# Kernel optimization log

Measured on AMD Instinct MI355X. Metric: run time of the kernel, lower is better.

## Reference

```python
import jax, jax.numpy as jnp
import numpy as np

N = 1_000_000
C = 128
B = 16  # number of instances (batch segments)
EPS = 1e-5


def setup_inputs() -> dict:
    key = jax.random.key(0)
    k1, k2 = jax.random.split(key)
    x = jax.random.normal(k1, (N, C), dtype=jnp.float32)
    batch_idx = jnp.sort(jax.random.randint(k2, (N,), 0, B, dtype=jnp.int32))
    weight = jnp.ones((1, C), dtype=jnp.float32)
    bias = jnp.zeros((1, C), dtype=jnp.float32)
    return {"x": x, "batch_idx": batch_idx, "weight": weight, "bias": bias}


def reference(x, batch_idx, weight, bias):
    # per-instance counts [B, 1]
    cnt = jax.ops.segment_sum(jnp.ones((x.shape[0], 1), x.dtype), batch_idx,
                              num_segments=B)
    cnt = jnp.maximum(cnt, 1.0)
    # segment mean [B, C]
    mean = jax.ops.segment_sum(x, batch_idx, num_segments=B) / cnt
    centered = x - mean[batch_idx]               # broadcast-add of -mean
    # segment mean of squared centered features -> per-instance variance [B, C]
    var = jax.ops.segment_sum(centered * centered, batch_idx, num_segments=B) / cnt
    instd = 1.0 / jnp.sqrt(var + EPS)            # [B, C]
    # broadcast-multiply, then affine
    return centered * instd[batch_idx] * weight + bias
```

## Files before the change

### kernel.cpp

```cpp
#include <hip/hip_runtime.h>

#define CC 128
#define BSEG 16
#define EPSV 1e-5f
#define ROWS_PER_BLOCK 512

__global__ __launch_bounds__(256) void ms_stats(const float* __restrict__ x,
                                                const int* __restrict__ bidx,
                                                int n,
                                                float* __restrict__ sum,
                                                float* __restrict__ sumsq,
                                                float* __restrict__ cnt)
{
    const int r0 = blockIdx.x * ROWS_PER_BLOCK;
    if (r0 >= n) return;
    const int rend = min(r0 + ROWS_PER_BLOCK, n);
    const int tq = threadIdx.x & 31;
    const int tr = threadIdx.x >> 5;

    const int seg_first = bidx[r0];
    const int seg_last  = bidx[rend - 1];

    float s0 = 0.f, s1 = 0.f, s2 = 0.f, s3 = 0.f;
    float q0 = 0.f, q1 = 0.f, q2 = 0.f, q3 = 0.f;

    if (seg_first == seg_last) {
        for (int r = r0 + tr; r < rend; r += 8) {
            const float4 v = *reinterpret_cast<const float4*>(x + (size_t)r * CC + tq * 4);
            s0 += v.x; s1 += v.y; s2 += v.z; s3 += v.w;
            q0 += v.x * v.x; q1 += v.y * v.y; q2 += v.z * v.z; q3 += v.w * v.w;
        }
        __shared__ float red[8][8][32];
        red[tr][0][tq] = s0; red[tr][1][tq] = s1; red[tr][2][tq] = s2; red[tr][3][tq] = s3;
        red[tr][4][tq] = q0; red[tr][5][tq] = q1; red[tr][6][tq] = q2; red[tr][7][tq] = q3;
        __syncthreads();
        const int j = threadIdx.x >> 5;
        float acc = 0.f;
        #pragma unroll
        for (int k = 0; k < 8; ++k) acc += red[k][j][tq];
        const int ch = tq * 4 + (j & 3);
        atomicAdd(((j < 4) ? sum : sumsq) + seg_first * CC + ch, acc);
        if (threadIdx.x == 0)
            atomicAdd(cnt + seg_first, (float)(rend - r0));
    } else {
        int cur = -1;
        float rows = 0.f;
        for (int r = r0 + tr; r < rend; r += 8) {
            const int seg = bidx[r];
            if (seg != cur) {
                if (cur >= 0) {
                    float* sd = sum   + cur * CC + tq * 4;
                    float* qd = sumsq + cur * CC + tq * 4;
                    atomicAdd(sd + 0, s0); atomicAdd(sd + 1, s1);
                    atomicAdd(sd + 2, s2); atomicAdd(sd + 3, s3);
                    atomicAdd(qd + 0, q0); atomicAdd(qd + 1, q1);
                    atomicAdd(qd + 2, q2); atomicAdd(qd + 3, q3);
                    if (tq == 0) atomicAdd(cnt + cur, rows);
                    s0 = s1 = s2 = s3 = q0 = q1 = q2 = q3 = 0.f;
                    rows = 0.f;
                }
                cur = seg;
            }
            const float4 v = *reinterpret_cast<const float4*>(x + (size_t)r * CC + tq * 4);
            s0 += v.x; s1 += v.y; s2 += v.z; s3 += v.w;
            q0 += v.x * v.x; q1 += v.y * v.y; q2 += v.z * v.z; q3 += v.w * v.w;
            rows += 1.f;
        }
        if (cur >= 0) {
            float* sd = sum   + cur * CC + tq * 4;
            float* qd = sumsq + cur * CC + tq * 4;
            atomicAdd(sd + 0, s0); atomicAdd(sd + 1, s1);
            atomicAdd(sd + 2, s2); atomicAdd(sd + 3, s3);
            atomicAdd(qd + 0, q0); atomicAdd(qd + 1, q1);
            atomicAdd(qd + 2, q2); atomicAdd(qd + 3, q3);
            if (tq == 0) atomicAdd(cnt + cur, rows);
        }
    }
}

__global__ __launch_bounds__(256) void ms_finalize(const float* __restrict__ sum,
                                                   const float* __restrict__ sumsq,
                                                   const float* __restrict__ cnt,
                                                   const float* __restrict__ w,
                                                   const float* __restrict__ bias,
                                                   float* __restrict__ scale,
                                                   float* __restrict__ shift)
{
    const int i = blockIdx.x * blockDim.x + threadIdx.x;
    if (i >= BSEG * CC) return;
    const int b = i / CC;
    const int c = i % CC;
    const float nn = fmaxf(cnt[b], 1.0f);
    const float mean = sum[i] / nn;
    const float var = fmaxf(sumsq[i] / nn - mean * mean, 0.0f);
    const float instd = rsqrtf(var + EPSV);
    const float sc = instd * w[c];
    scale[i] = sc;
    shift[i] = bias[c] - mean * sc;
}

__global__ __launch_bounds__(256) void ms_norm(const float* __restrict__ x,
                                               const int* __restrict__ bidx,
                                               const float* __restrict__ scale,
                                               const float* __restrict__ shift,
                                               float* __restrict__ out,
                                               int n)
{
    __shared__ float4 s_scale[BSEG * 32];
    __shared__ float4 s_shift[BSEG * 32];
    for (int i = threadIdx.x; i < BSEG * 32; i += blockDim.x) {
        s_scale[i] = reinterpret_cast<const float4*>(scale)[i];
        s_shift[i] = reinterpret_cast<const float4*>(shift)[i];
    }
    __syncthreads();

    const unsigned total = (unsigned)n * 32u;
    const unsigned stride = gridDim.x * blockDim.x;
    for (unsigned idx = blockIdx.x * blockDim.x + threadIdx.x; idx < total; idx += stride) {
        const int r = (int)(idx >> 5);
        const int q = (int)(idx & 31);
        const int seg = bidx[r];
        const float4 v  = reinterpret_cast<const float4*>(x)[idx];
        const float4 sc = s_scale[seg * 32 + q];
        const float4 sh = s_shift[seg * 32 + q];
        float4 o;
        o.x = fmaf(v.x, sc.x, sh.x);
        o.y = fmaf(v.y, sc.y, sh.y);
        o.z = fmaf(v.z, sc.z, sh.z);
        o.w = fmaf(v.w, sc.w, sh.w);
        reinterpret_cast<float4*>(out)[idx] = o;
    }
}

extern "C" void kernel_launch(void* const* d_in, const int* in_sizes, int n_in,
                              void* d_out, int out_size, void* d_ws, size_t ws_size,
                              hipStream_t stream)
{
    const float* x    = (const float*)d_in[0];
    const int*   bidx = (const int*)d_in[1];
    const float* w    = (const float*)d_in[2];
    const float* bias = (const float*)d_in[3];
    float* out = (float*)d_out;
    const int n = in_sizes[1];

    float* ws    = (float*)d_ws;
    float* sum   = ws;
    float* sumsq = ws + BSEG * CC;
    float* cnt   = ws + 2 * BSEG * CC;
    float* scale = ws + 2 * BSEG * CC + BSEG;
    float* shift = scale + BSEG * CC;

    hipMemsetAsync(d_ws, 0, (size_t)(2 * BSEG * CC + BSEG) * sizeof(float), stream);

    const int g1 = (n + ROWS_PER_BLOCK - 1) / ROWS_PER_BLOCK;
    ms_stats<<<g1, 256, 0, stream>>>(x, bidx, n, sum, sumsq, cnt);
    ms_finalize<<<(BSEG * CC + 255) / 256, 256, 0, stream>>>(sum, sumsq, cnt, w, bias, scale, shift);
    ms_norm<<<2048, 256, 0, stream>>>(x, bidx, scale, shift, out, n);
}
```

Before: 352.6 us.

## Fuse finalize into norm kernel, reverse traversal, use nontemporal stores

Drops the separate finalize kernel. Each norm block now recomputes the per-segment scale and shift into shared memory from the raw sums, which removes one launch and a global round trip. The norm loop walks rows in reverse so that the most recently read tail of x, likely still in cache after the stats pass, is consumed first. Output is written with nontemporal stores to avoid polluting the cache. The cost is that all 2048 blocks redo the 2048-element finalize, and shared-memory reads become scalar with possible bank conflicts.

```diff
diff --git a/kernel.cpp b/kernel.cpp
--- a/kernel.cpp
+++ b/kernel.cpp
@@ -4,6 +4,8 @@
 #define BSEG 16
 #define EPSV 1e-5f
 #define ROWS_PER_BLOCK 512
+
+typedef float v4f __attribute__((ext_vector_type(4)));
 
 __global__ __launch_bounds__(256) void ms_stats(const float* __restrict__ x,
                                                 const int* __restrict__ bidx,
@@ -26,7 +28,7 @@
 
     if (seg_first == seg_last) {
         for (int r = r0 + tr; r < rend; r += 8) {
-            const float4 v = *reinterpret_cast<const float4*>(x + (size_t)r * CC + tq * 4);
+            const v4f v = *reinterpret_cast<const v4f*>(x + (size_t)r * CC + tq * 4);
             s0 += v.x; s1 += v.y; s2 += v.z; s3 += v.w;
             q0 += v.x * v.x; q1 += v.y * v.y; q2 += v.z * v.z; q3 += v.w * v.w;
         }
@@ -61,7 +63,7 @@
                 }
                 cur = seg;
             }
-            const float4 v = *reinterpret_cast<const float4*>(x + (size_t)r * CC + tq * 4);
+            const v4f v = *reinterpret_cast<const v4f*>(x + (size_t)r * CC + tq * 4);
             s0 += v.x; s1 += v.y; s2 += v.z; s3 += v.w;
             q0 += v.x * v.x; q1 += v.y * v.y; q2 += v.z * v.z; q3 += v.w * v.w;
             rows += 1.f;
@@ -78,57 +80,45 @@
     }
 }
 
-__global__ __launch_bounds__(256) void ms_finalize(const float* __restrict__ sum,
-                                                   const float* __restrict__ sumsq,
-                                                   const float* __restrict__ cnt,
-                                                   const float* __restrict__ w,
-                                                   const float* __restrict__ bias,
-                                                   float* __restrict__ scale,
-                                                   float* __restrict__ shift)
-{
-    const int i = blockIdx.x * blockDim.x + threadIdx.x;
-    if (i >= BSEG * CC) return;
-    const int b = i / CC;
-    const int c = i % CC;
-    const float nn = fmaxf(cnt[b], 1.0f);
-    const float mean = sum[i] / nn;
-    const float var = fmaxf(sumsq[i] / nn - mean * mean, 0.0f);
-    const float instd = rsqrtf(var + EPSV);
-    const float sc = instd * w[c];
-    scale[i] = sc;
-    shift[i] = bias[c] - mean * sc;
-}
-
 __global__ __launch_bounds__(256) void ms_norm(const float* __restrict__ x,
                                                const int* __restrict__ bidx,
-                                               const float* __restrict__ scale,
-                                               const float* __restrict__ shift,
+                                               const float* __restrict__ sum,
+                                               const float* __restrict__ sumsq,
+                                               const float* __restrict__ cnt,
+                                               const float* __restrict__ w,
+                                               const float* __restrict__ bias,
                                                float* __restrict__ out,
                                                int n)
 {
-    __shared__ float4 s_scale[BSEG * 32];
-    __shared__ float4 s_shift[BSEG * 32];
-    for (int i = threadIdx.x; i < BSEG * 32; i += blockDim.x) {
-        s_scale[i] = reinterpret_cast<const float4*>(scale)[i];
-        s_shift[i] = reinterpret_cast<const float4*>(shift)[i];
+    __shared__ float s_scale[BSEG * CC];
+    __shared__ float s_shift[BSEG * CC];
+    for (int i = threadIdx.x; i < BSEG * CC; i += 256) {
+        const int b = i >> 7;
+        const int c = i & (CC - 1);
+        const float nn   = fmaxf(cnt[b], 1.0f);
+        const float mean = sum[i] / nn;
+        const float var  = fmaxf(sumsq[i] / nn - mean * mean, 0.0f);
+        const float sc   = rsqrtf(var + EPSV) * w[c];
+        s_scale[i] = sc;
+        s_shift[i] = fmaf(-mean, sc, bias[c]);
     }
     __syncthreads();
 
-    const unsigned total = (unsigned)n * 32u;
+    const unsigned total  = (unsigned)n * 32u;
     const unsigned stride = gridDim.x * blockDim.x;
-    for (unsigned idx = blockIdx.x * blockDim.x + threadIdx.x; idx < total; idx += stride) {
+    for (unsigned i = blockIdx.x * blockDim.x + threadIdx.x; i < total; i += stride) {
+        const unsigned idx = total - 1u - i;
         const int r = (int)(idx >> 5);
         const int q = (int)(idx & 31);
-        const int seg = bidx[r];
-        const float4 v  = reinterpret_cast<const float4*>(x)[idx];
-        const float4 sc = s_scale[seg * 32 + q];
-        const float4 sh = s_shift[seg * 32 + q];
-        float4 o;
-        o.x = fmaf(v.x, sc.x, sh.x);
-        o.y = fmaf(v.y, sc.y, sh.y);
-        o.z = fmaf(v.z, sc.z, sh.z);
-        o.w = fmaf(v.w, sc.w, sh.w);
-        reinterpret_cast<float4*>(out)[idx] = o;
+        const int seg  = bidx[r];
+        const int base = seg * CC + q * 4;
+        const v4f v = reinterpret_cast<const v4f*>(x)[idx];
+        v4f o;
+        o.x = fmaf(v.x, s_scale[base + 0], s_shift[base + 0]);
+        o.y = fmaf(v.y, s_scale[base + 1], s_shift[base + 1]);
+        o.z = fmaf(v.z, s_scale[base + 2], s_shift[base + 2]);
+        o.w = fmaf(v.w, s_scale[base + 3], s_shift[base + 3]);
+        __builtin_nontemporal_store(o, reinterpret_cast<v4f*>(out) + idx);
     }
 }
 
@@ -147,13 +137,10 @@
     float* sum   = ws;
     float* sumsq = ws + BSEG * CC;
     float* cnt   = ws + 2 * BSEG * CC;
-    float* scale = ws + 2 * BSEG * CC + BSEG;
-    float* shift = scale + BSEG * CC;
 
-    hipMemsetAsync(d_ws, 0, (size_t)(2 * BSEG * CC + BSEG) * sizeof(float), stream);
+    (void)hipMemsetAsync(d_ws, 0, (size_t)(2 * BSEG * CC + BSEG) * sizeof(float), stream);
 
     const int g1 = (n + ROWS_PER_BLOCK - 1) / ROWS_PER_BLOCK;
     ms_stats<<<g1, 256, 0, stream>>>(x, bidx, n, sum, sumsq, cnt);
-    ms_finalize<<<(BSEG * CC + 255) / 256, 256, 0, stream>>>(sum, sumsq, cnt, w, bias, scale, shift);
-    ms_norm<<<2048, 256, 0, stream>>>(x, bidx, scale, shift, out, n);
+    ms_norm<<<2048, 256, 0, stream>>>(x, bidx, sum, sumsq, cnt, w, bias, out, n);
 }
```

New measurement: 316.5 us. 1.11x faster.
